# Kernel tuning notes

Measured on AMD Instinct MI355X. Metric: run time of the kernel, lower is better.

The kernel has to match this reference:

```python
import jax, jax.numpy as jnp
import numpy as np


def setup_inputs() -> dict:
    key = jax.random.key(0)
    ks = jax.random.split(key, 6)
    B, M, H = 256, 64, 512
    memory_state = jax.random.normal(ks[0], (B, M, M, M), dtype=jnp.float32) * 0.02
    hidden_state = jax.random.normal(ks[1], (B, H), dtype=jnp.float32)
    role1 = jnp.tanh(jax.random.normal(ks[2], (B, M), dtype=jnp.float32))
    role2 = jnp.tanh(jax.random.normal(ks[3], (B, M), dtype=jnp.float32))
    filer = jnp.tanh(jax.random.normal(ks[4], (B, M), dtype=jnp.float32))
    W_gate = jax.random.normal(ks[5], (1, H), dtype=jnp.float32) * (1.0 / np.sqrt(H))
    b_gate = jnp.zeros((1,), dtype=jnp.float32)
    return {"memory_state": memory_state, "hidden_state": hidden_state,
            "role1": role1, "role2": role2, "filer": filer,
            "W_gate": W_gate, "b_gate": b_gate}


def reference(memory_state, hidden_state, role1, role2, filer, W_gate, b_gate):
    M = memory_state.shape[1]
    # write gate: sigmoid(Linear(h) + 1), shape [B, 1]
    write_gate = jax.nn.sigmoid(hidden_state @ W_gate.T + b_gate + 1.0)
    # outer product of roles: [B, M, M]
    role = jnp.einsum('br,bt->brt', role1, role2)
    # read from 3D associative memory: [B, M]
    prev_info = jnp.einsum('brt,brtf->bf', role, memory_state)
    cur_info = write_gate * (filer - prev_info)
    scale = 1.0 / M
    # gated outer-product write
    new_memory = memory_state + jnp.einsum('brt,bf->brtf', role, cur_info * scale)
    # norm-clip rescale
    mem_norm = jnp.linalg.norm(new_memory.reshape(new_memory.shape[0], -1), axis=-1)
    mem_norm = jax.nn.relu(mem_norm - 1.0) + 1.0
    new_memory = new_memory / mem_norm[:, None, None, None]
    return new_memory
```

## Files before the change

kernel.cpp:

```cpp
#include <hip/hip_runtime.h>
#include <math.h>

#define B 256
#define M 64
#define THREADS 1024
#define F4_PER_BATCH 65536
#define ITERS 64

typedef float f32x4 __attribute__((ext_vector_type(4)));

__device__ __forceinline__ float wave_sum64(float v) {
    #pragma unroll
    for (int m = 32; m >= 1; m >>= 1) v += __shfl_xor(v, m);
    return v;
}

__global__ __launch_bounds__(THREADS) void k_fused(
    const float* __restrict__ mem, const float* __restrict__ hidden,
    const float* __restrict__ role1, const float* __restrict__ role2,
    const float* __restrict__ filer, const float* __restrict__ W_gate,
    const float* __restrict__ b_gate, float* __restrict__ out)
{
    const int b   = blockIdx.x;
    const int tid = threadIdx.x;

    __shared__ float role_s[M * M];
    __shared__ float part[16][M];
    __shared__ float ss_lds[16];
    __shared__ float c2_s[M];
    __shared__ float inv_s;

    #pragma unroll
    for (int i = tid; i < M * M; i += THREADS)
        role_s[i] = role1[b * M + (i >> 6)] * role2[b * M + (i & 63)];
    __syncthreads();

    const float4* mem4 = (const float4*)(mem + (size_t)b * (M * M * M));

    float4 ap = make_float4(0.f, 0.f, 0.f, 0.f);
    float  ss = 0.f;
    #pragma unroll 8
    for (int i = 0; i < ITERS; ++i) {
        const int idx = i * THREADS + tid;
        const float4 v = mem4[idx];
        const float  r = role_s[idx >> 4];
        ap.x = fmaf(r, v.x, ap.x);
        ap.y = fmaf(r, v.y, ap.y);
        ap.z = fmaf(r, v.z, ap.z);
        ap.w = fmaf(r, v.w, ap.w);
        ss = fmaf(v.x, v.x, ss);
        ss = fmaf(v.y, v.y, ss);
        ss = fmaf(v.z, v.z, ss);
        ss = fmaf(v.w, v.w, ss);
    }

    #pragma unroll
    for (int m = 16; m <= 32; m <<= 1) {
        ap.x += __shfl_xor(ap.x, m);
        ap.y += __shfl_xor(ap.y, m);
        ap.z += __shfl_xor(ap.z, m);
        ap.w += __shfl_xor(ap.w, m);
    }
    const float ssw = wave_sum64(ss);

    const int wave = tid >> 6;
    const int lane = tid & 63;
    if (lane < 16) {
        part[wave][4 * lane + 0] = ap.x;
        part[wave][4 * lane + 1] = ap.y;
        part[wave][4 * lane + 2] = ap.z;
        part[wave][4 * lane + 3] = ap.w;
    }
    if (lane == 0) ss_lds[wave] = ssw;
    __syncthreads();

    if (tid < M) {
        const int f = tid;
        float p = 0.f;
        #pragma unroll
        for (int w = 0; w < 16; ++w) p += part[w][f];
        float ssm = 0.f;
        #pragma unroll
        for (int w = 0; w < 16; ++w) ssm += ss_lds[w];

        float g = 0.f;
        #pragma unroll
        for (int j = 0; j < 8; ++j) {
            const int i = f + j * 64;
            g = fmaf(hidden[(size_t)b * 512 + i], W_gate[i], g);
        }
        g = wave_sum64(g);
        g = 1.f / (1.f + expf(-(g + b_gate[0] + 1.f)));

        const float fil = filer[b * M + f];
        const float cur = g * (fil - p);

        const float d1   = wave_sum64(p * cur);
        const float ssc  = wave_sum64(cur * cur);
        const float r1   = role1[b * M + f];
        const float r2   = role2[b * M + f];
        const float ssr1 = wave_sum64(r1 * r1);
        const float ssr2 = wave_sum64(r2 * r2);

        const float sc = 1.0f / (float)M;
        const float ns = ssm + 2.f * sc * d1 + sc * sc * ssr1 * ssr2 * ssc;
        const float inv = 1.0f / fmaxf(sqrtf(ns), 1.0f);

        c2_s[f] = cur * sc * inv;
        if (f == 0) inv_s = inv;
    }
    __syncthreads();

    const float  inv = inv_s;
    const float4 c   = ((const float4*)c2_s)[tid & 15];
    f32x4* out4 = (f32x4*)(out + (size_t)b * (M * M * M));
    #pragma unroll 8
    for (int i = 0; i < ITERS; ++i) {
        const int idx = i * THREADS + tid;
        const float4 v = mem4[idx];
        const float  r = role_s[idx >> 4];
        f32x4 o;
        o.x = fmaf(r, c.x, v.x * inv);
        o.y = fmaf(r, c.y, v.y * inv);
        o.z = fmaf(r, c.z, v.z * inv);
        o.w = fmaf(r, c.w, v.w * inv);
        __builtin_nontemporal_store(o, &out4[idx]);
    }
}

extern "C" void kernel_launch(void* const* d_in, const int* in_sizes, int n_in,
                              void* d_out, int out_size, void* d_ws, size_t ws_size,
                              hipStream_t stream) {
    const float* mem    = (const float*)d_in[0];
    const float* hidden = (const float*)d_in[1];
    const float* role1  = (const float*)d_in[2];
    const float* role2  = (const float*)d_in[3];
    const float* filer  = (const float*)d_in[4];
    const float* Wg     = (const float*)d_in[5];
    const float* bg     = (const float*)d_in[6];
    float* out = (float*)d_out;

    hipLaunchKernelGGL(k_fused, dim3(B), dim3(THREADS), 0, stream,
                       mem, hidden, role1, role2, filer, Wg, bg, out);
}
```

Baseline: 132.9 us.

## Split fused kernel into three pipelined launches overlapping reduce and write halves

Replaces the single 256-block kernel (one 1024-thread block per batch) with three kernels of 256-thread blocks, each handling a 1/8 slice of a batch's memory. The first launch reduces the first half of the batches into workspace partials. The second interleaves writing the first half with reducing the second half, and the third writes the second half. This is meant to raise parallelism beyond 256 blocks and overlap the read-only and read-write phases. It adds two launch boundaries and workspace round trips, and each gate computation is repeated per slice.

```diff
diff --git a/kernel.cpp b/kernel.cpp
--- a/kernel.cpp
+++ b/kernel.cpp
@@ -1,11 +1,7 @@
 #include <hip/hip_runtime.h>
 #include <math.h>
 
-#define B 256
 #define M 64
-#define THREADS 1024
-#define F4_PER_BATCH 65536
-#define ITERS 64
 
 typedef float f32x4 __attribute__((ext_vector_type(4)));
 
@@ -15,35 +11,32 @@
     return v;
 }
 
-__global__ __launch_bounds__(THREADS) void k_fused(
-    const float* __restrict__ mem, const float* __restrict__ hidden,
-    const float* __restrict__ role1, const float* __restrict__ role2,
-    const float* __restrict__ filer, const float* __restrict__ W_gate,
-    const float* __restrict__ b_gate, float* __restrict__ out)
-{
-    const int b   = blockIdx.x;
+__device__ __forceinline__ void reduce_part(
+    const float* __restrict__ mem, const float* __restrict__ role1,
+    const float* __restrict__ role2, float* __restrict__ prev_part,
+    float* __restrict__ ss_part, int b, int sp)
+{
+    __shared__ float  role_r[512];
+    __shared__ float4 part[4][16];
+    __shared__ float  ss_lds[4];
     const int tid = threadIdx.x;
 
-    __shared__ float role_s[M * M];
-    __shared__ float part[16][M];
-    __shared__ float ss_lds[16];
-    __shared__ float c2_s[M];
-    __shared__ float inv_s;
-
-    #pragma unroll
-    for (int i = tid; i < M * M; i += THREADS)
-        role_s[i] = role1[b * M + (i >> 6)] * role2[b * M + (i & 63)];
+    for (int i = tid; i < 512; i += 256) {
+        const int rt = sp * 512 + i;
+        role_r[i] = role1[b * M + (rt >> 6)] * role2[b * M + (rt & 63)];
+    }
     __syncthreads();
 
-    const float4* mem4 = (const float4*)(mem + (size_t)b * (M * M * M));
+    const float4* mem4 = (const float4*)(mem + (size_t)b * 262144);
+    const int f4 = tid & 15, rsub = tid >> 4;
 
     float4 ap = make_float4(0.f, 0.f, 0.f, 0.f);
     float  ss = 0.f;
     #pragma unroll 8
-    for (int i = 0; i < ITERS; ++i) {
-        const int idx = i * THREADS + tid;
-        const float4 v = mem4[idx];
-        const float  r = role_s[idx >> 4];
+    for (int i = 0; i < 32; ++i) {
+        const int lrt = rsub + i * 16;
+        const float4 v = mem4[(size_t)(sp * 512 + lrt) * 16 + f4];
+        const float  r = role_r[lrt];
         ap.x = fmaf(r, v.x, ap.x);
         ap.y = fmaf(r, v.y, ap.y);
         ap.z = fmaf(r, v.z, ap.z);
@@ -63,38 +56,54 @@
     }
     const float ssw = wave_sum64(ss);
 
-    const int wave = tid >> 6;
-    const int lane = tid & 63;
-    if (lane < 16) {
-        part[wave][4 * lane + 0] = ap.x;
-        part[wave][4 * lane + 1] = ap.y;
-        part[wave][4 * lane + 2] = ap.z;
-        part[wave][4 * lane + 3] = ap.w;
-    }
+    const int wave = tid >> 6, lane = tid & 63;
+    if (lane < 16) part[wave][lane] = ap;
     if (lane == 0) ss_lds[wave] = ssw;
     __syncthreads();
+
+    if (tid < 16) {
+        float4 a0 = part[0][tid], a1 = part[1][tid], a2 = part[2][tid], a3 = part[3][tid];
+        float4 s;
+        s.x = (a0.x + a1.x) + (a2.x + a3.x);
+        s.y = (a0.y + a1.y) + (a2.y + a3.y);
+        s.z = (a0.z + a1.z) + (a2.z + a3.z);
+        s.w = (a0.w + a1.w) + (a2.w + a3.w);
+        ((float4*)prev_part)[(size_t)(b * 8 + sp) * 16 + tid] = s;
+    }
+    if (tid == 0)
+        ss_part[b * 8 + sp] = (ss_lds[0] + ss_lds[1]) + (ss_lds[2] + ss_lds[3]);
+}
+
+__device__ __forceinline__ void write_part(
+    const float* __restrict__ mem, const float* __restrict__ hidden,
+    const float* __restrict__ role1, const float* __restrict__ role2,
+    const float* __restrict__ filer, const float* __restrict__ W_gate,
+    const float* __restrict__ b_gate, const float* __restrict__ prev_part,
+    const float* __restrict__ ss_part, float* __restrict__ out, int b, int ck)
+{
+    __shared__ float role_w[512];
+    __shared__ float c2_s[M];
+    __shared__ float inv_s;
+    const int tid = threadIdx.x;
 
     if (tid < M) {
         const int f = tid;
         float p = 0.f;
         #pragma unroll
-        for (int w = 0; w < 16; ++w) p += part[w][f];
+        for (int s = 0; s < 8; ++s) p += prev_part[(size_t)(b * 8 + s) * M + f];
         float ssm = 0.f;
         #pragma unroll
-        for (int w = 0; w < 16; ++w) ssm += ss_lds[w];
+        for (int s = 0; s < 8; ++s) ssm += ss_part[b * 8 + s];
 
         float g = 0.f;
         #pragma unroll
-        for (int j = 0; j < 8; ++j) {
-            const int i = f + j * 64;
-            g = fmaf(hidden[(size_t)b * 512 + i], W_gate[i], g);
-        }
+        for (int j = 0; j < 8; ++j)
+            g = fmaf(hidden[(size_t)b * 512 + f + j * 64], W_gate[f + j * 64], g);
         g = wave_sum64(g);
         g = 1.f / (1.f + expf(-(g + b_gate[0] + 1.f)));
 
         const float fil = filer[b * M + f];
         const float cur = g * (fil - p);
-
         const float d1   = wave_sum64(p * cur);
         const float ssc  = wave_sum64(cur * cur);
         const float r1   = role1[b * M + f];
@@ -105,20 +114,27 @@
         const float sc = 1.0f / (float)M;
         const float ns = ssm + 2.f * sc * d1 + sc * sc * ssr1 * ssr2 * ssc;
         const float inv = 1.0f / fmaxf(sqrtf(ns), 1.0f);
-
         c2_s[f] = cur * sc * inv;
         if (f == 0) inv_s = inv;
     }
+    for (int i = tid; i < 512; i += 256) {
+        const int rt = ck * 512 + i;
+        role_w[i] = role1[b * M + (rt >> 6)] * role2[b * M + (rt & 63)];
+    }
     __syncthreads();
 
     const float  inv = inv_s;
     const float4 c   = ((const float4*)c2_s)[tid & 15];
-    f32x4* out4 = (f32x4*)(out + (size_t)b * (M * M * M));
+    const float4* mem4 = (const float4*)(mem + (size_t)b * 262144);
+    f32x4* out4 = (f32x4*)(out + (size_t)b * 262144);
+    const int f4 = tid & 15, rsub = tid >> 4;
+
     #pragma unroll 8
-    for (int i = 0; i < ITERS; ++i) {
-        const int idx = i * THREADS + tid;
+    for (int i = 0; i < 32; ++i) {
+        const int lrt = rsub + i * 16;
+        const int idx = (ck * 512 + lrt) * 16 + f4;
         const float4 v = mem4[idx];
-        const float  r = role_s[idx >> 4];
+        const float  r = role_w[lrt];
         f32x4 o;
         o.x = fmaf(r, c.x, v.x * inv);
         o.y = fmaf(r, c.y, v.y * inv);
@@ -126,6 +142,42 @@
         o.w = fmaf(r, c.w, v.w * inv);
         __builtin_nontemporal_store(o, &out4[idx]);
     }
+}
+
+__global__ __launch_bounds__(256) void kA(
+    const float* __restrict__ mem, const float* __restrict__ role1,
+    const float* __restrict__ role2, float* __restrict__ prev_part,
+    float* __restrict__ ss_part)
+{
+    reduce_part(mem, role1, role2, prev_part, ss_part,
+                blockIdx.x >> 3, blockIdx.x & 7);
+}
+
+__global__ __launch_bounds__(256) void kB(
+    const float* __restrict__ mem, const float* __restrict__ hidden,
+    const float* __restrict__ role1, const float* __restrict__ role2,
+    const float* __restrict__ filer, const float* __restrict__ W_gate,
+    const float* __restrict__ b_gate, float* __restrict__ prev_part,
+    float* __restrict__ ss_part, float* __restrict__ out)
+{
+    const int sub = blockIdx.x >> 1;
+    if (blockIdx.x & 1)
+        write_part(mem, hidden, role1, role2, filer, W_gate, b_gate,
+                   prev_part, ss_part, out, sub >> 3, sub & 7);
+    else
+        reduce_part(mem, role1, role2, prev_part, ss_part,
+                    128 + (sub >> 3), sub & 7);
+}
+
+__global__ __launch_bounds__(256) void kC(
+    const float* __restrict__ mem, const float* __restrict__ hidden,
+    const float* __restrict__ role1, const float* __restrict__ role2,
+    const float* __restrict__ filer, const float* __restrict__ W_gate,
+    const float* __restrict__ b_gate, const float* __restrict__ prev_part,
+    const float* __restrict__ ss_part, float* __restrict__ out)
+{
+    write_part(mem, hidden, role1, role2, filer, W_gate, b_gate,
+               prev_part, ss_part, out, 128 + (blockIdx.x >> 3), blockIdx.x & 7);
 }
 
 extern "C" void kernel_launch(void* const* d_in, const int* in_sizes, int n_in,
@@ -140,6 +192,16 @@
     const float* bg     = (const float*)d_in[6];
     float* out = (float*)d_out;
 
-    hipLaunchKernelGGL(k_fused, dim3(B), dim3(THREADS), 0, stream,
-                       mem, hidden, role1, role2, filer, Wg, bg, out);
-}
+    float* ws        = (float*)d_ws;
+    float* prev_part = ws;
+    float* ss_part   = ws + 131072;
+
+    hipLaunchKernelGGL(kA, dim3(1024), dim3(256), 0, stream,
+                       mem, role1, role2, prev_part, ss_part);
+    hipLaunchKernelGGL(kB, dim3(2048), dim3(256), 0, stream,
+                       mem, hidden, role1, role2, filer, Wg, bg,
+                       prev_part, ss_part, out);
+    hipLaunchKernelGGL(kC, dim3(1024), dim3(256), 0, stream,
+                       mem, hidden, role1, role2, filer, Wg, bg,
+                       prev_part, ss_part, out);
+}
```

Result: slower. 144.3 us (+8.6%).
